# Kernel optimization log

Hardware: AMD Instinct MI355X
Metric: run time of the kernel (lower is better)

## Reference

```python
import jax, jax.numpy as jnp
import numpy as np
import math

DIM = 1024
HEADS = 16
WINDOW = 256  # window_size; also used as block size (band covers 3 blocks)


def _rope(x):
    # canonical half-split RoPE over the FULL feature dim (as the module applies
    # it before the head split), base 10000
    b, s, d = x.shape
    half = d // 2
    inv_freq = 1.0 / (10000.0 ** (jnp.arange(half, dtype=jnp.float32) / half))
    ang = jnp.arange(s, dtype=jnp.float32)[:, None] * inv_freq[None, :]  # [s, half]
    cos, sin = jnp.cos(ang), jnp.sin(ang)
    x1, x2 = x[..., :half], x[..., half:]
    return jnp.concatenate([x1 * cos - x2 * sin, x1 * sin + x2 * cos], axis=-1)


def setup_inputs() -> dict:
    key = jax.random.key(0)
    ks = jax.random.split(key, 8)
    d = DIM
    q = jax.random.normal(ks[0], (2, 4096, d), dtype=jnp.float32)
    k = jax.random.normal(ks[1], (2, 4096, d), dtype=jnp.float32)
    v = jax.random.normal(ks[2], (2, 4096, d), dtype=jnp.float32)
    wq = jax.random.normal(ks[3], (d, d), dtype=jnp.float32) * 0.02
    wk = jax.random.normal(ks[4], (d, d), dtype=jnp.float32) * 0.02
    wv = jax.random.normal(ks[5], (d, d), dtype=jnp.float32) * 0.02
    wo_w = jax.random.normal(ks[6], (d, d), dtype=jnp.float32) * 0.02
    wo_b = jnp.zeros((d,), dtype=jnp.float32)
    return {"q": q, "k": k, "v": v, "wq": wq, "wk": wk, "wv": wv,
            "wo_w": wo_w, "wo_b": wo_b}


def reference(q, k, v, wq, wk, wv, wo_w, wo_b):
    b, s, d = q.shape
    h, W = HEADS, WINDOW
    dk = d // h
    B = W                      # block size == window -> band of 3 blocks
    nb = s // B

    # projections (torch Linear: x @ W^T), then RoPE over the full dim
    qp = _rope(jnp.einsum('bsd,ed->bse', q, wq))
    kp = _rope(jnp.einsum('bsd,ed->bse', k, wk))
    vp = jnp.einsum('bsd,ed->bse', v, wv)

    # split heads -> [b, h, s, dk]
    qh = qp.reshape(b, s, h, dk).transpose(0, 2, 1, 3)
    kh = kp.reshape(b, s, h, dk).transpose(0, 2, 1, 3)
    vh = vp.reshape(b, s, h, dk).transpose(0, 2, 1, 3)

    # pad keys/values by one block on each side, gather 3-block bands
    kpad = jnp.pad(kh, ((0, 0), (0, 0), (B, B), (0, 0)))
    vpad = jnp.pad(vh, ((0, 0), (0, 0), (B, B), (0, 0)))
    kblk = kpad.reshape(b, h, nb + 2, B, dk)
    vblk = vpad.reshape(b, h, nb + 2, B, dk)
    kband = jnp.concatenate([kblk[:, :, i:i + nb] for i in range(3)], axis=3)  # [b,h,nb,3B,dk]
    vband = jnp.concatenate([vblk[:, :, i:i + nb] for i in range(3)], axis=3)

    qb = qh.reshape(b, h, nb, B, dk)
    # NOTE: original multiplies by sqrt(dim_k) (not divides) -- kept faithfully
    scores = jnp.einsum('bhnqd,bhnkd->bhnqk', qb, kband) * math.sqrt(dk)

    # band mask: key global pos = (n-1)*B + ki, query global pos = n*B + qi
    n_idx = jnp.arange(nb)[:, None, None]
    qi = jnp.arange(B)[None, :, None]
    ki = jnp.arange(3 * B)[None, None, :]
    kpos = (n_idx - 1) * B + ki
    rel = ki - B - qi  # key_pos - query_pos
    valid = (rel >= -W) & (rel <= W) & (kpos >= 0) & (kpos < s)  # [nb,B,3B]

    neg = jnp.asarray(jnp.finfo(scores.dtype).min, scores.dtype)
    scores = jnp.where(valid[None, None], scores, neg)
    attn = jax.nn.softmax(scores, axis=-1)

    out = jnp.einsum('bhnqk,bhnkd->bhnqd', attn, vband)
    out = out.reshape(b, h, s, dk).transpose(0, 2, 1, 3).reshape(b, s, d)
    return jnp.einsum('bsd,ed->bse', out, wo_w) + wo_b
```

## Files before the change

### kernel.cpp

```cpp
#include <hip/hip_runtime.h>


typedef __attribute__((ext_vector_type(8))) short short8v;
typedef __attribute__((ext_vector_type(4))) float float4v;
typedef __attribute__((ext_vector_type(8))) _Float16 half8v;

#define MFMA_BF16(A_, B_, C_) __builtin_amdgcn_mfma_f32_16x16x32_bf16((A_), (B_), (C_), 0, 0, 0)
#define MFMA_F16(A_, B_, C_)  __builtin_amdgcn_mfma_f32_16x16x32_f16((A_), (B_), (C_), 0, 0, 0)

#define VMW_(n) asm volatile("s_waitcnt vmcnt(" #n ")" ::: "memory")
#define VMW(n) VMW_(n)
#define LGKM0 asm volatile("s_waitcnt lgkmcnt(0)" ::: "memory")
#define BARF do { __builtin_amdgcn_s_barrier(); asm volatile("" ::: "memory"); } while (0)

__device__ __forceinline__ void split_rn(float x, short& h, short& l) {
    unsigned int u = __float_as_uint(x);
    u += 0x7fffu + ((u >> 16) & 1u);
    unsigned int hb = u & 0xffff0000u;
    h = (short)(hb >> 16);
    float lo = x - __uint_as_float(hb);
    l = (short)(__float_as_uint(lo) >> 16);
}

__device__ __forceinline__ void dma16(const void* g, void* l) {
    __builtin_amdgcn_global_load_lds(
        (__attribute__((address_space(1))) void*)g,
        (__attribute__((address_space(3))) void*)l, 16, 0, 0);
}

__global__ __launch_bounds__(256) void prep_k(
    const float* __restrict__ wq, const float* __restrict__ wk,
    const float* __restrict__ wv, unsigned short* __restrict__ scr)
{
    const int M1 = 1 << 20;
    unsigned int tid = blockIdx.x * 256 + threadIdx.x;
    if (tid < (unsigned)M1) {
        short h, l; split_rn(wq[tid], h, l);
        scr[tid] = (unsigned short)h;
        scr[M1 + tid] = (unsigned short)l;
    } else if (tid < (unsigned)(2 * M1)) {
        unsigned int i = tid - M1;
        short h, l; split_rn(wk[i], h, l);
        scr[2 * M1 + i] = (unsigned short)h;
        scr[3 * M1 + i] = (unsigned short)l;
    } else {
        unsigned int i = tid - 2 * M1;
        scr[4 * M1 + i] = __builtin_bit_cast(unsigned short, (_Float16)wv[i]);
    }
}

__global__ __launch_bounds__(512, 2) void gemm_qk2(
    const float* __restrict__ A0, const short* __restrict__ Bh0,
    const short* __restrict__ Bl0, float* __restrict__ C0,
    const float* __restrict__ A1, const short* __restrict__ Bh1,
    const short* __restrict__ Bl1, float* __restrict__ C1)
{
    __shared__ __align__(16) short S[2 * 32768];

    const int bid = blockIdx.x;
    const int cid = ((bid & 7) << 5) | (bid >> 3);
    const int z   = cid >> 7;
    const int rem = cid & 127;
    const int bm  = (rem >> 2) << 8;
    const int bn  = (rem & 3) << 8;

    const float* Ap  = z ? A1  : A0;
    const short* Bhp = z ? Bh1 : Bh0;
    const short* Blp = z ? Bl1 : Bl0;
    float*       Cp  = z ? C1  : C0;

    const int t = threadIdx.x;
    const int wave = t >> 6, lane = t & 63;
    const int c16 = lane & 15, quad = lane >> 4;
    const int wm = (wave >> 2) << 7;
    const int wn = (wave & 3) << 6;

    const int ar = t >> 1;
    const int ah16 = (t & 1) << 4;
    const int fA = (ar & 3) ^ ((ar >> 2) & 3);
    const int swA0 = ((((t & 1) << 1) | 0) ^ fA) << 3;
    const int swA1 = ((((t & 1) << 1) | 1) ^ fA) << 3;

    const int br  = lane >> 2;
    const int fsl = (((lane & 3) ^ ((br & 3) ^ ((br >> 2) & 3))) << 3);

    const int frd = ((quad ^ ((c16 & 3) ^ ((c16 >> 2) & 3))) << 3);

    float4v acc[8][4];
#pragma unroll
    for (int i = 0; i < 8; i++)
#pragma unroll
        for (int j = 0; j < 4; j++) acc[i][j] = (float4v){0.f, 0.f, 0.f, 0.f};

#define STAGE_B(pp, kk)                                                          \
    do {                                                                         \
        const size_t rb = (size_t)(bn + (wave << 5) + br) * 1024 + (kk) + fsl;   \
        short* dh = S + (pp) * 32768 + 16384 + (wave << 10);                     \
        short* dl = dh + 8192;                                                   \
        dma16(Bhp + rb,             dh);                                         \
        dma16(Bhp + rb + 16 * 1024, dh + 512);                                   \
        dma16(Blp + rb,             dl);                                         \
        dma16(Blp + rb + 16 * 1024, dl + 512);                                   \
    } while (0)

    const float* arow = Ap + (size_t)(bm + ar) * 1024 + ah16;
    float4v ap0 = *(const float4v*)(arow + 0);
    float4v ap1 = *(const float4v*)(arow + 4);
    float4v ap2 = *(const float4v*)(arow + 8);
    float4v ap3 = *(const float4v*)(arow + 12);
    STAGE_B(0, 0);

#define SPLIT_WRITE(sp_)                                                         \
    do {                                                                         \
        short8v h0, l0, h1, l1;                                                  \
        _Pragma("unroll")                                                        \
        for (int jj = 0; jj < 4; jj++) {                                         \
            short hh, ll;                                                        \
            split_rn(ap0[jj], hh, ll); h0[jj] = hh;     l0[jj] = ll;             \
            split_rn(ap1[jj], hh, ll); h0[jj + 4] = hh; l0[jj + 4] = ll;         \
            split_rn(ap2[jj], hh, ll); h1[jj] = hh;     l1[jj] = ll;             \
            split_rn(ap3[jj], hh, ll); h1[jj + 4] = hh; l1[jj + 4] = ll;         \
        }                                                                        \
        short* abase = (sp_) + ar * 32;                                          \
        *(short8v*)(abase + swA0) = h0;                                          \
        *(short8v*)(abase + swA1) = h1;                                          \
        *(short8v*)(abase + 8192 + swA0) = l0;                                   \
        *(short8v*)(abase + 8192 + swA1) = l1;                                   \
    } while (0)

#define LOAD_AH_BH(sp_)                                                          \
    _Pragma("unroll")                                                            \
    for (int i = 0; i < 8; i++)                                                  \
        ah[i] = *(const short8v*)((sp_) + (wm + i * 16 + c16) * 32 + frd);       \
    _Pragma("unroll")                                                            \
    for (int j = 0; j < 4; j++)                                                  \
        bh[j] = *(const short8v*)((sp_) + 16384 + (wn + j * 16 + c16) * 32 + frd)

#define MFMA_CLUSTER(AARR, BARR)                                                 \
    do {                                                                         \
        __builtin_amdgcn_s_setprio(1);                                           \
        _Pragma("unroll")                                                        \
        for (int i = 0; i < 8; i++)                                              \
            _Pragma("unroll")                                                    \
            for (int j = 0; j < 4; j++)                                          \
                acc[i][j] = MFMA_BF16(AARR[i & 7], BARR[j & 3], acc[i][j]);      \
        __builtin_amdgcn_s_setprio(0);                                           \
    } while (0)

    int kb = 0;
#pragma unroll 1
    for (int tt = 0; tt < 31; ++tt, kb += 32) {
        const int p = tt & 1;
        short* sp = S + p * 32768;

        VMW(4);
        SPLIT_WRITE(sp);
        ap0 = *(const float4v*)(arow + kb + 32);
        ap1 = *(const float4v*)(arow + kb + 36);
        ap2 = *(const float4v*)(arow + kb + 40);
        ap3 = *(const float4v*)(arow + kb + 44);
        LGKM0;
        BARF;
        STAGE_B(p ^ 1, kb + 32);
        VMW(10);
        BARF;
        short8v ah[8], bh[4];
        LOAD_AH_BH(sp);
        MFMA_CLUSTER(ah, bh);
        VMW(8);
        BARF;
        {
            short8v bl[4];
#pragma unroll
            for (int j = 0; j < 4; j++)
                bl[j] = *(const short8v*)(sp + 24576 + (wn + j * 16 + c16) * 32 + frd);
            MFMA_CLUSTER(ah, bl);
        }
        {
            short8v al[8];
#pragma unroll
            for (int i = 0; i < 8; i++)
                al[i] = *(const short8v*)(sp + 8192 + (wm + i * 16 + c16) * 32 + frd);
            MFMA_CLUSTER(al, bh);
        }
    }

    {
        short* sp = S + 32768;
        VMW(4);
        SPLIT_WRITE(sp);
        LGKM0;
        BARF;
        VMW(2);
        BARF;
        short8v ah[8], bh[4];
        LOAD_AH_BH(sp);
        MFMA_CLUSTER(ah, bh);
        VMW(0);
        BARF;
        {
            short8v bl[4];
#pragma unroll
            for (int j = 0; j < 4; j++)
                bl[j] = *(const short8v*)(sp + 24576 + (wn + j * 16 + c16) * 32 + frd);
            MFMA_CLUSTER(ah, bl);
        }
        {
            short8v al[8];
#pragma unroll
            for (int i = 0; i < 8; i++)
                al[i] = *(const short8v*)(sp + 8192 + (wm + i * 16 + c16) * 32 + frd);
            MFMA_CLUSTER(al, bh);
        }
    }

#undef STAGE_B
#undef SPLIT_WRITE
#undef LOAD_AH_BH
#undef MFMA_CLUSTER

#pragma unroll
    for (int i = 0; i < 8; i++) {
        const size_t gr0 = (size_t)(bm + wm + i * 16 + quad * 4);
#pragma unroll
        for (int j = 0; j < 4; j++) {
            const int gc = bn + wn + j * 16 + c16;
#pragma unroll
            for (int r = 0; r < 4; r++)
                Cp[(gr0 + r) * 1024 + gc] = acc[i][j][r];
        }
    }
}

template <int AF16, int BF16, int OMODE>
__global__ __launch_bounds__(256) void gemm16(
    const void* __restrict__ Ap, const void* __restrict__ Bp,
    void* __restrict__ Cp, const float* __restrict__ bias)
{
    const int N = 1024, K = 1024;

    __shared__ __align__(16) short As[128 * 32];
    __shared__ __align__(16) short Bs[128 * 32];

    const int t = threadIdx.x;
    const int bm = blockIdx.y << 7;
    const int bn = blockIdx.x << 7;
    const int lane = t & 63;
    const int wave = t >> 6;
    const int wm = (wave >> 1) << 6;
    const int wn = (wave & 1) << 6;
    const int c16 = lane & 15;
    const int quad = lane >> 4;
    const int lr = t >> 2;
    const int lc = (t & 3) << 3;

    float4v acc[4][4];
#pragma unroll
    for (int i = 0; i < 4; i++)
#pragma unroll
        for (int j = 0; j < 4; j++) acc[i][j] = (float4v){0.f, 0.f, 0.f, 0.f};

    for (int kb = 0; kb < K; kb += 32) {
        if (AF16) {
            const _Float16* Af = (const _Float16*)Ap;
#pragma unroll
            for (int g = 0; g < 2; g++)
                dma16(Af + (size_t)(bm + g * 64 + lr) * K + kb + lc,
                      As + g * 2048 + wave * 512);
        } else {
            const float* Af = (const float*)Ap;
#pragma unroll
            for (int g = 0; g < 2; g++) {
                const float* src = Af + (size_t)(bm + g * 64 + lr) * K + kb + lc;
                float4v f0 = *(const float4v*)src;
                float4v f1 = *(const float4v*)(src + 4);
                half8v h;
#pragma unroll
                for (int j = 0; j < 8; j++) h[j] = (_Float16)((j < 4) ? f0[j] : f1[j - 4]);
                *(half8v*)(As + (g * 64 + lr) * 32 + lc) = h;
            }
        }
        if (BF16) {
            const _Float16* Bf = (const _Float16*)Bp;
#pragma unroll
            for (int g = 0; g < 2; g++)
                dma16(Bf + (size_t)(bn + g * 64 + lr) * K + kb + lc,
                      Bs + g * 2048 + wave * 512);
        } else {
            const float* Bf = (const float*)Bp;
#pragma unroll
            for (int g = 0; g < 2; g++) {
                const float* src = Bf + (size_t)(bn + g * 64 + lr) * K + kb + lc;
                float4v f0 = *(const float4v*)src;
                float4v f1 = *(const float4v*)(src + 4);
                half8v h;
#pragma unroll
                for (int j = 0; j < 8; j++) h[j] = (_Float16)((j < 4) ? f0[j] : f1[j - 4]);
                *(half8v*)(Bs + (g * 64 + lr) * 32 + lc) = h;
            }
        }
        __syncthreads();

        half8v ah[4], bh[4];
#pragma unroll
        for (int i = 0; i < 4; i++)
            ah[i] = *(const half8v*)(As + (wm + i * 16 + c16) * 32 + quad * 8);
#pragma unroll
        for (int j = 0; j < 4; j++)
            bh[j] = *(const half8v*)(Bs + (wn + j * 16 + c16) * 32 + quad * 8);
#pragma unroll
        for (int i = 0; i < 4; i++)
#pragma unroll
            for (int j = 0; j < 4; j++)
                acc[i][j] = MFMA_F16(ah[i], bh[j], acc[i][j]);
        __syncthreads();
    }

#pragma unroll
    for (int i = 0; i < 4; i++)
#pragma unroll
        for (int j = 0; j < 4; j++)
#pragma unroll
            for (int r = 0; r < 4; r++) {
                int gr = bm + wm + i * 16 + quad * 4 + r;
                int gc = bn + wn + j * 16 + c16;
                float vv = acc[i][j][r];
                if (OMODE == 0) {
                    ((unsigned short*)Cp)[((size_t)(gc << 1) + (gr >> 12)) * 4096 + (gr & 4095)] =
                        __builtin_bit_cast(unsigned short, (_Float16)vv);
                } else {
                    ((float*)Cp)[(size_t)gr * N + gc] = vv + bias[gc];
                }
            }
}

__global__ __launch_bounds__(256) void rope_pack(float* __restrict__ QP, float* __restrict__ KP)
{
    int sp = blockIdx.x;
    int t = threadIdx.x;
    float* rows[4] = { QP + ((size_t)sp << 10), QP + ((size_t)(4096 + sp) << 10),
                       KP + ((size_t)sp << 10), KP + ((size_t)(4096 + sp) << 10) };

    float c[2], sn[2];
    float x1[4][2], x2[4][2];
#pragma unroll
    for (int p = 0; p < 2; p++) {
        int j = t + p * 256;
        float freq = __expf(-0.017988946f * (float)j);
        float ang = (float)sp * freq;
        sincosf(ang, &sn[p], &c[p]);
#pragma unroll
        for (int r = 0; r < 4; r++) {
            x1[r][p] = rows[r][j];
            x2[r][p] = rows[r][j + 512];
        }
    }
    __syncthreads();
#pragma unroll
    for (int r = 0; r < 4; r++) {
        unsigned short* u = (unsigned short*)rows[r];
#pragma unroll
        for (int p = 0; p < 2; p++) {
            int j = t + p * 256;
            float y1 = x1[r][p] * c[p] - x2[r][p] * sn[p];
            float y2 = x1[r][p] * sn[p] + x2[r][p] * c[p];
            short h1, l1, h2, l2;
            split_rn(y1, h1, l1);
            split_rn(y2, h2, l2);
            u[j] = (unsigned short)h1;
            u[j + 512] = (unsigned short)h2;
            u[1024 + j] = (unsigned short)l1;
            u[1024 + j + 512] = (unsigned short)l2;
        }
    }
}

__global__ __launch_bounds__(256) void attn_k(
    const unsigned short* __restrict__ QHL, const unsigned short* __restrict__ KHL,
    const unsigned short* __restrict__ VT, unsigned short* __restrict__ AO)
{
    const int S = 4096;
    const float NEG = -1e30f;
    const float PSC = 512.0f;
    const int bq = blockIdx.x, h = blockIdx.y, b = blockIdx.z;
    const int t = threadIdx.x;
    const int wave = t >> 6, lane = t & 63;
    const int col = lane & 15, quad = lane >> 4;
    const int qg = (bq << 6) + (wave << 4);

    __shared__ __align__(16) short Khs[64 * 72];
    __shared__ __align__(16) short Kls[64 * 72];
    __shared__ __align__(16) short Vs[64 * 72];
    __shared__ __align__(16) short Ps[4][16 * 72];
    short* myP = &Ps[wave][0];

    const int sk = t >> 3;
    const int sd = (t & 7) << 3;

    short8v qh[2], ql[2];
    {
        const unsigned short* qr = QHL + ((size_t)(b * S + qg + col) << 11) + h * 64 + quad * 8;
        qh[0] = *(const short8v*)(qr);
        qh[1] = *(const short8v*)(qr + 32);
        ql[0] = *(const short8v*)(qr + 1024);
        ql[1] = *(const short8v*)(qr + 1024 + 32);
    }

    float mrun[4], lrun[4];
    float4v O[4];
#pragma unroll
    for (int r = 0; r < 4; r++) { mrun[r] = NEG; lrun[r] = 0.f; }
#pragma unroll
    for (int t4 = 0; t4 < 4; t4++) O[t4] = (float4v){0.f, 0.f, 0.f, 0.f};

    const int blk0 = bq << 6;
    const int kstart = (blk0 - 256 > 0) ? (blk0 - 256) : 0;
    const int kend = (blk0 + 320 < S) ? (blk0 + 320) : S;

    for (int kb = kstart; kb < kend; kb += 64) {
#pragma unroll
        for (int p = 0; p < 2; p++) {
            int key = p * 32 + sk;
            const unsigned short* krow = KHL + ((size_t)(b * S + kb + key) << 11) + h * 64 + sd;
            *(short8v*)(Khs + key * 72 + sd) = *(const short8v*)krow;
            *(short8v*)(Kls + key * 72 + sd) = *(const short8v*)(krow + 1024);
            int dm = p * 32 + sk;
            const unsigned short* vrow = VT + ((size_t)((h * 64 + dm) << 1) + b) * S + kb + sd;
            *(short8v*)(Vs + dm * 72 + sd) = *(const short8v*)vrow;
        }
        __syncthreads();

        float4v sv[4];
#pragma unroll
        for (int c = 0; c < 4; c++) {
            const short* kro = Khs + (c * 16 + col) * 72 + quad * 8;
            const short* klo = Kls + (c * 16 + col) * 72 + quad * 8;
            short8v kh0 = *(const short8v*)kro;
            short8v kh1 = *(const short8v*)(kro + 32);
            short8v kl0 = *(const short8v*)klo;
            short8v kl1 = *(const short8v*)(klo + 32);
            float4v sc = (float4v){0.f, 0.f, 0.f, 0.f};
            sc = MFMA_BF16(qh[0], kh0, sc);
            sc = MFMA_BF16(qh[1], kh1, sc);
            sc = MFMA_BF16(qh[0], kl0, sc);
            sc = MFMA_BF16(qh[1], kl1, sc);
            sc = MFMA_BF16(ql[0], kh0, sc);
            sc = MFMA_BF16(ql[1], kh1, sc);
            sv[c] = sc;
        }

        float mx[4], alpha[4], psum[4];
#pragma unroll
        for (int r = 0; r < 4; r++) {
            int qrow = qg + quad * 4 + r;
            float m = NEG;
#pragma unroll
            for (int c = 0; c < 4; c++) {
                int key = kb + c * 16 + col;
                float vv = (key >= qrow - 256 && key <= qrow + 256) ? sv[c][r] * 8.0f : NEG;
                sv[c][r] = vv;
                m = fmaxf(m, vv);
            }
            mx[r] = m;
        }
#pragma unroll
        for (int st = 1; st < 16; st <<= 1)
#pragma unroll
            for (int r = 0; r < 4; r++) mx[r] = fmaxf(mx[r], __shfl_xor(mx[r], st, 64));

#pragma unroll
        for (int r = 0; r < 4; r++) {
            float mn = fmaxf(mrun[r], mx[r]);
            alpha[r] = __expf(mrun[r] - mn);
            mrun[r] = mn;
            float ps = 0.f;
#pragma unroll
            for (int c = 0; c < 4; c++) {
                float p = __expf(sv[c][r] - mn);
                ps += p;
                myP[(quad * 4 + r) * 72 + c * 16 + col] =
                    __builtin_bit_cast(short, (_Float16)(p * PSC));
            }
            psum[r] = ps;
        }
#pragma unroll
        for (int st = 1; st < 16; st <<= 1)
#pragma unroll
            for (int r = 0; r < 4; r++) psum[r] += __shfl_xor(psum[r], st, 64);
#pragma unroll
        for (int r = 0; r < 4; r++) lrun[r] = lrun[r] * alpha[r] + psum[r];
#pragma unroll
        for (int t4 = 0; t4 < 4; t4++)
#pragma unroll
            for (int r = 0; r < 4; r++) O[t4][r] *= alpha[r];

#pragma unroll
        for (int kf = 0; kf < 2; kf++) {
            half8v pa = *(const half8v*)(myP + col * 72 + kf * 32 + quad * 8);
#pragma unroll
            for (int t4 = 0; t4 < 4; t4++) {
                half8v vb = *(const half8v*)(Vs + (t4 * 16 + col) * 72 + kf * 32 + quad * 8);
                O[t4] = MFMA_F16(pa, vb, O[t4]);
            }
        }
        __syncthreads();
    }

#pragma unroll
    for (int r = 0; r < 4; r++) {
        float inv = (lrun[r] > 0.f) ? (1.0f / (lrun[r] * PSC)) : 0.f;
        unsigned short* orow = AO + (size_t)(b * S + qg + quad * 4 + r) * 1024 + h * 64;
#pragma unroll
        for (int t4 = 0; t4 < 4; t4++)
            orow[t4 * 16 + col] = __builtin_bit_cast(unsigned short, (_Float16)(O[t4][r] * inv));
    }
}

extern "C" void kernel_launch(void* const* d_in, const int* in_sizes, int n_in,
                              void* d_out, int out_size, void* d_ws, size_t ws_size,
                              hipStream_t stream) {
    const float* q   = (const float*)d_in[0];
    const float* k   = (const float*)d_in[1];
    const float* v   = (const float*)d_in[2];
    const float* wq  = (const float*)d_in[3];
    const float* wk  = (const float*)d_in[4];
    const float* wv  = (const float*)d_in[5];
    const float* wo  = (const float*)d_in[6];
    const float* wob = (const float*)d_in[7];

    float* QP = (float*)d_ws;
    float* KP = QP + (size_t)8192 * 1024;
    unsigned short* VT = (unsigned short*)(KP + (size_t)8192 * 1024);
    unsigned short* AO = VT + (size_t)8192 * 1024;

    unsigned short* scr = (unsigned short*)d_out;
    const int M1 = 1 << 20;
    const short* wqh = (const short*)(scr);
    const short* wql = (const short*)(scr + M1);
    const short* wkh = (const short*)(scr + 2 * M1);
    const short* wkl = (const short*)(scr + 3 * M1);
    const void*  wv16 = (const void*)(scr + 4 * M1);

    prep_k<<<12288, 256, 0, stream>>>(wq, wk, wv, scr);
    gemm_qk2<<<256, 512, 0, stream>>>(q, wqh, wql, QP, k, wkh, wkl, KP);
    rope_pack<<<4096, 256, 0, stream>>>(QP, KP);
    gemm16<0, 1, 0><<<dim3(8, 64), 256, 0, stream>>>(v, wv16, (void*)VT, nullptr);
    attn_k<<<dim3(64, 16, 2), 256, 0, stream>>>((const unsigned short*)QP,
                                                (const unsigned short*)KP, VT, AO);
    gemm16<1, 0, 1><<<dim3(8, 64), 256, 0, stream>>>(AO, wo, d_out, wob);
}
```

Before: 429.7 us.

## Restructure split-bf16 GEMM main loop to one barrier and overlapped A split

```diff
diff --git a/kernel.cpp b/kernel.cpp
--- a/kernel.cpp
+++ b/kernel.cpp
@@ -12,6 +12,7 @@
 #define VMW(n) VMW_(n)
 #define LGKM0 asm volatile("s_waitcnt lgkmcnt(0)" ::: "memory")
 #define BARF do { __builtin_amdgcn_s_barrier(); asm volatile("" ::: "memory"); } while (0)
+#define FENCE asm volatile("" ::: "memory")
 
 __device__ __forceinline__ void split_rn(float x, short& h, short& l) {
     unsigned int u = __float_as_uint(x);
@@ -103,13 +104,6 @@
         dma16(Blp + rb + 16 * 1024, dl + 512);                                   \
     } while (0)
 
-    const float* arow = Ap + (size_t)(bm + ar) * 1024 + ah16;
-    float4v ap0 = *(const float4v*)(arow + 0);
-    float4v ap1 = *(const float4v*)(arow + 4);
-    float4v ap2 = *(const float4v*)(arow + 8);
-    float4v ap3 = *(const float4v*)(arow + 12);
-    STAGE_B(0, 0);
-
 #define SPLIT_WRITE(sp_)                                                         \
     do {                                                                         \
         short8v h0, l0, h1, l1;                                                  \
@@ -128,14 +122,6 @@
         *(short8v*)(abase + 8192 + swA1) = l1;                                   \
     } while (0)
 
-#define LOAD_AH_BH(sp_)                                                          \
-    _Pragma("unroll")                                                            \
-    for (int i = 0; i < 8; i++)                                                  \
-        ah[i] = *(const short8v*)((sp_) + (wm + i * 16 + c16) * 32 + frd);       \
-    _Pragma("unroll")                                                            \
-    for (int j = 0; j < 4; j++)                                                  \
-        bh[j] = *(const short8v*)((sp_) + 16384 + (wn + j * 16 + c16) * 32 + frd)
-
 #define MFMA_CLUSTER(AARR, BARR)                                                 \
     do {                                                                         \
         __builtin_amdgcn_s_setprio(1);                                           \
@@ -147,76 +133,102 @@
         __builtin_amdgcn_s_setprio(0);                                           \
     } while (0)
 
+    const float* arow = Ap + (size_t)(bm + ar) * 1024 + ah16;
+    float4v ap0 = *(const float4v*)(arow + 0);
+    float4v ap1 = *(const float4v*)(arow + 4);
+    float4v ap2 = *(const float4v*)(arow + 8);
+    float4v ap3 = *(const float4v*)(arow + 12);
+    FENCE;
+    STAGE_B(0, 0);
+    VMW(4);
+    SPLIT_WRITE(S);
+    FENCE;
+    ap0 = *(const float4v*)(arow + 32);
+    ap1 = *(const float4v*)(arow + 36);
+    ap2 = *(const float4v*)(arow + 40);
+    ap3 = *(const float4v*)(arow + 44);
+    LGKM0;
+
     int kb = 0;
 #pragma unroll 1
     for (int tt = 0; tt < 31; ++tt, kb += 32) {
-        const int p = tt & 1;
-        short* sp = S + p * 32768;
+        short* sp = S + (tt & 1) * 32768;
+        short* sn = S + ((tt & 1) ^ 1) * 32768;
+
+        STAGE_B((tt & 1) ^ 1, kb + 32);
+        VMW(8);
+        BARF;
+
+        short8v ahv[8], bhv[4];
+#pragma unroll
+        for (int i = 0; i < 8; i++)
+            ahv[i] = *(const short8v*)(sp + (wm + i * 16 + c16) * 32 + frd);
+#pragma unroll
+        for (int j = 0; j < 4; j++)
+            bhv[j] = *(const short8v*)(sp + 16384 + (wn + j * 16 + c16) * 32 + frd);
+        MFMA_CLUSTER(ahv, bhv);
+
+        {
+            short8v blv[4];
+#pragma unroll
+            for (int j = 0; j < 4; j++)
+                blv[j] = *(const short8v*)(sp + 24576 + (wn + j * 16 + c16) * 32 + frd);
+            MFMA_CLUSTER(ahv, blv);
+        }
 
         VMW(4);
-        SPLIT_WRITE(sp);
-        ap0 = *(const float4v*)(arow + kb + 32);
-        ap1 = *(const float4v*)(arow + kb + 36);
-        ap2 = *(const float4v*)(arow + kb + 40);
-        ap3 = *(const float4v*)(arow + kb + 44);
+        SPLIT_WRITE(sn);
+        FENCE;
+        {
+            int kn = kb + 64;
+            if (kn >= 1024) kn = 0;
+            ap0 = *(const float4v*)(arow + kn);
+            ap1 = *(const float4v*)(arow + kn + 4);
+            ap2 = *(const float4v*)(arow + kn + 8);
+            ap3 = *(const float4v*)(arow + kn + 12);
+        }
+
+        {
+            short8v alv[8];
+#pragma unroll
+            for (int i = 0; i < 8; i++)
+                alv[i] = *(const short8v*)(sp + 8192 + (wm + i * 16 + c16) * 32 + frd);
+            MFMA_CLUSTER(alv, bhv);
+        }
         LGKM0;
         BARF;
-        STAGE_B(p ^ 1, kb + 32);
-        VMW(10);
-        BARF;
-        short8v ah[8], bh[4];
-        LOAD_AH_BH(sp);
-        MFMA_CLUSTER(ah, bh);
-        VMW(8);
-        BARF;
-        {
-            short8v bl[4];
-#pragma unroll
-            for (int j = 0; j < 4; j++)
-                bl[j] = *(const short8v*)(sp + 24576 + (wn + j * 16 + c16) * 32 + frd);
-            MFMA_CLUSTER(ah, bl);
-        }
-        {
-            short8v al[8];
-#pragma unroll
-            for (int i = 0; i < 8; i++)
-                al[i] = *(const short8v*)(sp + 8192 + (wm + i * 16 + c16) * 32 + frd);
-            MFMA_CLUSTER(al, bh);
-        }
     }
 
     {
         short* sp = S + 32768;
         VMW(4);
-        SPLIT_WRITE(sp);
-        LGKM0;
         BARF;
-        VMW(2);
-        BARF;
-        short8v ah[8], bh[4];
-        LOAD_AH_BH(sp);
-        MFMA_CLUSTER(ah, bh);
-        VMW(0);
-        BARF;
+        short8v ahv[8], bhv[4];
+#pragma unroll
+        for (int i = 0; i < 8; i++)
+            ahv[i] = *(const short8v*)(sp + (wm + i * 16 + c16) * 32 + frd);
+#pragma unroll
+        for (int j = 0; j < 4; j++)
+            bhv[j] = *(const short8v*)(sp + 16384 + (wn + j * 16 + c16) * 32 + frd);
+        MFMA_CLUSTER(ahv, bhv);
         {
-            short8v bl[4];
+            short8v blv[4];
 #pragma unroll
             for (int j = 0; j < 4; j++)
-                bl[j] = *(const short8v*)(sp + 24576 + (wn + j * 16 + c16) * 32 + frd);
-            MFMA_CLUSTER(ah, bl);
+                blv[j] = *(const short8v*)(sp + 24576 + (wn + j * 16 + c16) * 32 + frd);
+            MFMA_CLUSTER(ahv, blv);
         }
         {
-            short8v al[8];
+            short8v alv[8];
 #pragma unroll
             for (int i = 0; i < 8; i++)
-                al[i] = *(const short8v*)(sp + 8192 + (wm + i * 16 + c16) * 32 + frd);
-            MFMA_CLUSTER(al, bh);
+                alv[i] = *(const short8v*)(sp + 8192 + (wm + i * 16 + c16) * 32 + frd);
+            MFMA_CLUSTER(alv, bhv);
         }
     }
 
 #undef STAGE_B
 #undef SPLIT_WRITE
-#undef LOAD_AH_BH
 #undef MFMA_CLUSTER
 
 #pragma unroll
```

Result: faster. 419.1 us (-2.5%).
